# Kernel tuning notes

Measured on AMD Instinct MI355X. Metric: run time of the kernel, lower is better.

Reference implementation:

```python
import math
import jax, jax.numpy as jnp
import numpy as np

B, H, T, N, DV = 2, 8, 2048, 512, 128
THETA = 2.0 ** 16
TWO_PI = 2.0 * math.pi


def _get_freqs(n, theta):
    # quantize(arange(n), q=2): floor(t/2)*2, so each pair shares a frequency
    t = np.floor(np.arange(n, dtype=np.float32) / 2.0) * 2.0
    return (1.0 / theta ** (t / n) / TWO_PI).astype(np.float32)


def setup_inputs() -> dict:
    key = jax.random.key(0)
    k1, k2 = jax.random.split(key)
    Q = jax.random.normal(k1, (B, H, T, N), dtype=jnp.float32)
    V = jax.random.normal(k2, (B, H, T, DV), dtype=jnp.float32)
    freqs = jnp.asarray(_get_freqs(N, THETA)).reshape(1, 1, 1, N)
    return {"Q": Q, "V": V, "freqs": freqs}


def _rotate_half_interleaved(v):
    # stack((-v[..., 1::2], v[..., ::2]), -1).reshape(v.shape)
    v2 = v.reshape(*v.shape[:-1], -1, 2)
    rot = jnp.stack((-v2[..., 1], v2[..., 0]), axis=-1)
    return rot.reshape(v.shape)


def reference(Q, V, freqs):
    t = Q.shape[2]
    # phases: [1,1,T,N]
    phases = jnp.arange(t, dtype=jnp.float32).reshape(1, 1, t, 1) * freqs
    phases = (phases % 1.0) * TWO_PI
    cos, sin = jnp.cos(phases), jnp.sin(phases)
    QR = Q * cos + _rotate_half_interleaved(Q) * sin  # KR = QR (K is Q)
    scores = jnp.einsum('bhtn,bhsn->bhts', QR, QR)
    scores = jnp.tril(scores, k=-1)  # strictly lower triangular, no softmax
    return jnp.einsum('bhts,bhsd->bhtd', scores, V)
```

## Files before the change

### kernel.cpp

```cpp
#include <hip/hip_runtime.h>
#include <hip/hip_bf16.h>
#include <stdint.h>

#define T_DIM 2048
#define N_DIM 512
#define DV_DIM 128
#define NH 16

typedef __bf16 bf16x8 __attribute__((ext_vector_type(8)));
typedef float f32x4 __attribute__((ext_vector_type(4)));
typedef float f32x2 __attribute__((ext_vector_type(2)));
typedef unsigned int u32x2 __attribute__((ext_vector_type(2)));
typedef unsigned int u32x4 __attribute__((ext_vector_type(4)));

__device__ __forceinline__ unsigned bf16rne(float x) {
  unsigned u = __builtin_bit_cast(unsigned, x);
  return (u + 0x7FFFu + ((u >> 16) & 1u)) >> 16;
}

__device__ __forceinline__ void load_lds16(const void* g, void* l) {
  __builtin_amdgcn_global_load_lds((const __attribute__((address_space(1))) void*)g,
                                   (__attribute__((address_space(3))) void*)l, 16, 0, 0);
}

__global__ __launch_bounds__(256, 2)
void prep_kernel(const float* __restrict__ Q, const float* __restrict__ freqs,
                 const float* __restrict__ V,
                 unsigned int* __restrict__ qrOut,
                 unsigned int* __restrict__ qrTOut,
                 unsigned short* __restrict__ vt32) {
  __shared__ unsigned int smem32[2112];
  const int bid = blockIdx.x;
  const int tid = threadIdx.x;

  if (bid < 4096) {
    auto tile32 = reinterpret_cast<unsigned int(*)[33]>(smem32);
    const unsigned short* tile16 = reinterpret_cast<const unsigned short*>(smem32);
    const int k = bid >> 3;
    const int bh = (bid & 7) + 8 * (k & 1);
    const int rest = k >> 1;
    const int tt = rest >> 3;
    const int nn = rest & 7;
    const int t0 = tt * 64, n0 = nn * 64;

    const int c2 = tid & 31;
    const int r0 = tid >> 5;
    const float f = freqs[n0 + 2 * c2];

    const float* src = Q + ((size_t)bh * T_DIM + t0) * N_DIM + n0 + 2 * c2;
    f32x2 qv[8];
#pragma unroll
    for (int it = 0; it < 8; ++it)
      qv[it] = *(const f32x2*)(src + (size_t)(it * 8 + r0) * N_DIM);

    unsigned int* qrb = qrOut + ((size_t)bh * T_DIM + t0) * 256 + (n0 >> 1) + c2;
#pragma unroll
    for (int it = 0; it < 8; ++it) {
      int r = it * 8 + r0;
      float ph = (float)(t0 + r) * f;
      ph = ph - floorf(ph);
      float sn = __builtin_amdgcn_sinf(ph);
      float cn = __builtin_amdgcn_cosf(ph);
      unsigned lo = bf16rne(qv[it].x * cn - qv[it].y * sn);
      unsigned hi = bf16rne(qv[it].y * cn + qv[it].x * sn);
      unsigned pk = lo | (hi << 16);
      qrb[(size_t)r * 256] = pk;
      tile32[r][c2] = pk;
    }
    __syncthreads();
    unsigned int* dstb = qrTOut + ((size_t)bh * N_DIM + n0) * 1024 + (t0 >> 1);
#pragma unroll
    for (int it = 0; it < 8; ++it) {
      int slot = it * 256 + tid;
      int rn = slot >> 5;
      int c2r = slot & 31;
      unsigned lo = tile16[(2 * c2r) * 66 + rn];
      unsigned hi = tile16[(2 * c2r + 1) * 66 + rn];
      dstb[(size_t)rn * 1024 + c2r] = lo | (hi << 16);
    }
  } else {
    auto tile = reinterpret_cast<unsigned short(*)[128]>(smem32);
    const int vb = bid - 4096;
    const int bh = (vb & 7) + 8 * ((vb >> 3) & 1);
    const int sb = vb >> 4;
    const float* src = V + ((size_t)bh * T_DIM + sb * 32) * DV_DIM;
    f32x4 vv[4];
#pragma unroll
    for (int i = 0; i < 4; ++i)
      vv[i] = *(const f32x4*)(src + (size_t)(i * 1024 + tid * 4));
#pragma unroll
    for (int i = 0; i < 4; ++i) {
      int idx4 = i * 256 + tid;
      int row = idx4 >> 5;
      int col4 = idx4 & 31;
      u32x2 pk;
      pk[0] = bf16rne(vv[i][0]) | (bf16rne(vv[i][1]) << 16);
      pk[1] = bf16rne(vv[i][2]) | (bf16rne(vv[i][3]) << 16);
      *(u32x2*)&tile[row][col4 * 4] = pk;
    }
    __syncthreads();
    unsigned short* dst = vt32 + ((size_t)bh * 64 + sb) * 4096;
#pragma unroll
    for (int jj = 0; jj < 2; ++jj) {
      int j = jj * 256 + tid;
      int df = j >> 6, ln = j & 63;
      int lh2 = ln & 15, lg2 = ln >> 4;
      unsigned short tmp[8];
#pragma unroll
      for (int i = 0; i < 8; ++i) tmp[i] = tile[8 * lg2 + i][16 * df + lh2];
      *(u32x4*)(dst + j * 8) = *(u32x4*)tmp;
    }
  }
}

__global__ __launch_bounds__(256, 1)
void hprefix_kernel(const unsigned short* __restrict__ qrT,
                    const unsigned short* __restrict__ vt,
                    unsigned short* __restrict__ H) {
  const int bid = blockIdx.x;
  const int bh = (bid & 7) + 8 * ((bid >> 3) & 1);
  const int slab = bid >> 4;
  const int nsl = slab >> 2;
  const int dsl = slab & 3;
  const int tid = threadIdx.x;
  const int w = tid >> 6;
  const int lane = tid & 63;
  const int lh = lane & 15, lg = lane >> 4;

  const unsigned short* qrT_h = qrT + (size_t)bh * (N_DIM * T_DIM);
  const unsigned short* vt_h = vt + (size_t)bh * (64 * 4096);
  unsigned short* H_h = H + (size_t)bh * (16 * 65536);

  const f32x4 fzero = {0.f, 0.f, 0.f, 0.f};
  f32x4 acc00 = fzero, acc01 = fzero, acc10 = fzero, acc11 = fzero;

  for (int ch = 0; ch < 16; ++ch) {
#pragma unroll
    for (int nf = 0; nf < 2; ++nf)
#pragma unroll
      for (int dfl = 0; dfl < 2; ++dfl) {
        const f32x4 a = (nf == 0) ? (dfl == 0 ? acc00 : acc01)
                                  : (dfl == 0 ? acc10 : acc11);
        int nloc = w * 32 + nf * 16 + 4 * lg;
        int nblk = nsl * 4 + (nloc >> 5);
        int lg2 = (nloc >> 3) & 3;
        int i0 = nloc & 7;
        int df = dsl * 2 + dfl;
        int slot = df * 64 + lg2 * 16 + lh;
        u32x2 pk;
        pk[0] = bf16rne(a[0]) | (bf16rne(a[1]) << 16);
        pk[1] = bf16rne(a[2]) | (bf16rne(a[3]) << 16);
        *(u32x2*)(H_h + (size_t)ch * 65536 + nblk * 4096 + slot * 8 + i0) = pk;
      }
#pragma unroll
    for (int ks = 0; ks < 4; ++ks) {
      u32x4 a0, a1, b0, b1;
      {
        const unsigned short* pa = qrT_h + (size_t)(nsl * 128 + w * 32 + lh) * T_DIM
                                   + ch * 128 + ks * 32 + lg * 8;
        a0 = *(const u32x4*)pa;
        a1 = *(const u32x4*)(pa + 16 * T_DIM);
        const unsigned short* pb = vt_h + (size_t)(ch * 4 + ks) * 4096
                                   + ((dsl * 2) * 64 + lane) * 8;
        b0 = *(const u32x4*)pb;
        b1 = *(const u32x4*)(pb + 512);
      }
      acc00 = __builtin_amdgcn_mfma_f32_16x16x32_bf16(__builtin_bit_cast(bf16x8, a0), __builtin_bit_cast(bf16x8, b0), acc00, 0, 0, 0);
      acc01 = __builtin_amdgcn_mfma_f32_16x16x32_bf16(__builtin_bit_cast(bf16x8, a0), __builtin_bit_cast(bf16x8, b1), acc01, 0, 0, 0);
      acc10 = __builtin_amdgcn_mfma_f32_16x16x32_bf16(__builtin_bit_cast(bf16x8, a1), __builtin_bit_cast(bf16x8, b0), acc10, 0, 0, 0);
      acc11 = __builtin_amdgcn_mfma_f32_16x16x32_bf16(__builtin_bit_cast(bf16x8, a1), __builtin_bit_cast(bf16x8, b1), acc11, 0, 0, 0);
    }
  }
}

__global__ __launch_bounds__(512, 1)
void chunk_kernel(const unsigned short* __restrict__ qr,
                  const unsigned short* __restrict__ vt,
                  const unsigned short* __restrict__ H,
                  float* __restrict__ out) {
  __shared__ unsigned short kh_lds[2][16384];
  __shared__ unsigned short p_lds[8 * 2048];

  const int tid = threadIdx.x;
  const int w = tid >> 6;
  const int lane = tid & 63;
  const int lh = lane & 15, lg = lane >> 4;

  const int bid = blockIdx.x;
  const int head = (bid & 7) + 8 * ((bid >> 3) & 1);
  const int ch = bid >> 4;

  const unsigned short* qr_h = qr + (size_t)head * (T_DIM * N_DIM);
  const unsigned short* vt_h = vt + (size_t)head * (64 * 4096);
  const unsigned short* H_c = H + ((size_t)head * 16 + ch) * 65536;
  float* out_h = out + (size_t)head * (T_DIM * DV_DIM);

  const int tq = w * 16;
  const int tb = ch * 128 + tq;
  const int nsb = (w >> 1) + 1;

  u32x4 qf[16];
  {
    const unsigned short* pq = qr_h + (size_t)(tb + lh) * N_DIM + lg * 8;
#pragma unroll
    for (int ks = 0; ks < 16; ++ks) qf[ks] = *(const u32x4*)(pq + ks * 32);
  }

  int koff[4];
#pragma unroll
  for (int it = 0; it < 4; ++it) {
    int j = it * 512 + tid;
    int f = j >> 6, l = j & 63;
    int st = f >> 4, ks = f & 15;
    koff[it] = (st * 16 + (l & 15)) * 1024 + ks * 64 + (l >> 4) * 16;
  }
  auto stageK = [&](int sb, int buf) {
    const char* kb = (const char*)qr_h + ((size_t)ch * 128 + sb * 32) * 1024;
#pragma unroll
    for (int it = 0; it < 4; ++it)
      load_lds16(kb + koff[it], (char*)&kh_lds[buf][0] + (it * 512 + tid) * 16);
  };
  auto stageH = [&](int q, int buf) {
#pragma unroll
    for (int it = 0; it < 4; ++it) {
      int s = it * 512 + tid;
      int nb = s >> 7;
      int dfp = (s >> 6) & 1;
      int l = s & 63;
      const unsigned short* src = H_c + nb * 4096 + (2 * q + dfp) * 512 + l * 8;
      load_lds16(src, (char*)&kh_lds[buf][0] + s * 16);
    }
  };

  stageK(0, 0);
  stageK(1, 1);

  const f32x4 fzero = {0.f, 0.f, 0.f, 0.f};
  f32x4 o[8];
#pragma unroll
  for (int df = 0; df < 8; ++df) o[df] = fzero;

  for (int sb = 0; sb < 4; ++sb) {
    asm volatile("s_waitcnt vmcnt(4)" ::: "memory");
    __builtin_amdgcn_s_barrier();
    __builtin_amdgcn_sched_barrier(0);

    if (sb < nsb) {
      f32x4 sA = fzero, sB = fzero;
      const unsigned short* kbuf = &kh_lds[sb & 1][0];
#pragma unroll
      for (int ks = 0; ks < 16; ++ks) {
        bf16x8 kf0 = *(const bf16x8*)(kbuf + ks * 512 + lane * 8);
        bf16x8 kf1 = *(const bf16x8*)(kbuf + (16 + ks) * 512 + lane * 8);
        bf16x8 qb = __builtin_bit_cast(bf16x8, qf[ks]);
        sA = __builtin_amdgcn_mfma_f32_16x16x32_bf16(kf0, qb, sA, 0, 0, 0);
        sB = __builtin_amdgcn_mfma_f32_16x16x32_bf16(kf1, qb, sB, 0, 0, 0);
      }
      const int tloc = tq + lh;
#pragma unroll
      for (int r = 0; r < 4; ++r) {
        if (sb * 32 + 4 * lg + r >= tloc) sA[r] = 0.f;
        if (sb * 32 + 16 + 4 * lg + r >= tloc) sB[r] = 0.f;
      }
      u32x2 pkA, pkB;
      pkA[0] = bf16rne(sA[0]) | (bf16rne(sA[1]) << 16);
      pkA[1] = bf16rne(sA[2]) | (bf16rne(sA[3]) << 16);
      pkB[0] = bf16rne(sB[0]) | (bf16rne(sB[1]) << 16);
      pkB[1] = bf16rne(sB[2]) | (bf16rne(sB[3]) << 16);
      const int sa_in = 4 * lg;
      const int sb_in = 16 + 4 * lg;
      *(u32x2*)&p_lds[w * 2048 + sb * 512 + ((sa_in >> 3) * 16 + lh) * 8 + (sa_in & 7)] = pkA;
      *(u32x2*)&p_lds[w * 2048 + sb * 512 + ((sb_in >> 3) * 16 + lh) * 8 + (sb_in & 7)] = pkB;
    }

    asm volatile("s_waitcnt lgkmcnt(0)" ::: "memory");
    __builtin_amdgcn_sched_barrier(0);
    __builtin_amdgcn_s_barrier();

    if (sb == 0) stageK(2, 0);
    else if (sb == 1) stageK(3, 1);
    else if (sb == 2) stageH(0, 0);
  }
  stageH(1, 1);

  for (int f = 0; f < nsb; ++f) {
    bf16x8 pa = *(const bf16x8*)&p_lds[w * 2048 + f * 512 + lane * 8];
    const unsigned short* vb = vt_h + (size_t)(ch * 4 + f) * 4096 + lane * 8;
#pragma unroll
    for (int df = 0; df < 8; ++df) {
      bf16x8 vf = *(const bf16x8*)(vb + df * 512);
      o[df] = __builtin_amdgcn_mfma_f32_16x16x32_bf16(pa, vf, o[df], 0, 0, 0);
    }
  }

  for (int q = 0; q < 4; ++q) {
    if (q < 3) asm volatile("s_waitcnt vmcnt(4)" ::: "memory");
    else       asm volatile("s_waitcnt vmcnt(0)" ::: "memory");
    __builtin_amdgcn_s_barrier();
    __builtin_amdgcn_sched_barrier(0);

    const unsigned short* hbuf = &kh_lds[q & 1][0];
#pragma unroll
    for (int ks = 0; ks < 16; ++ks) {
      bf16x8 qa = __builtin_bit_cast(bf16x8, qf[ks]);
      bf16x8 hf0 = *(const bf16x8*)(hbuf + ks * 1024 + lane * 8);
      bf16x8 hf1 = *(const bf16x8*)(hbuf + ks * 1024 + 512 + lane * 8);
      o[2 * q] = __builtin_amdgcn_mfma_f32_16x16x32_bf16(qa, hf0, o[2 * q], 0, 0, 0);
      o[2 * q + 1] = __builtin_amdgcn_mfma_f32_16x16x32_bf16(qa, hf1, o[2 * q + 1], 0, 0, 0);
    }

    asm volatile("s_waitcnt lgkmcnt(0)" ::: "memory");
    __builtin_amdgcn_sched_barrier(0);
    __builtin_amdgcn_s_barrier();

    if (q < 2) stageH(q + 2, q & 1);
  }

  float* ob = out_h + (size_t)(tb + 4 * lg) * DV_DIM + lh;
#pragma unroll
  for (int df = 0; df < 8; ++df)
#pragma unroll
    for (int r = 0; r < 4; ++r)
      ob[(size_t)r * DV_DIM + df * 16] = o[df][r];
}

extern "C" void kernel_launch(void* const* d_in, const int* in_sizes, int n_in,
                              void* d_out, int out_size, void* d_ws, size_t ws_size,
                              hipStream_t stream) {
  const float* Q = (const float*)d_in[0];
  const float* V = (const float*)d_in[1];
  const float* freqs = (const float*)d_in[2];
  float* out = (float*)d_out;

  unsigned short* qr = (unsigned short*)d_ws;
  unsigned short* qrT = qr + (size_t)16777216;
  unsigned short* vt = qrT + (size_t)16777216;
  unsigned short* H = vt + (size_t)4194304;

  hipLaunchKernelGGL(prep_kernel, dim3(5120), dim3(256), 0, stream,
                     Q, freqs, V, (unsigned int*)qr, (unsigned int*)qrT, vt);
  hipLaunchKernelGGL(hprefix_kernel, dim3(256), dim3(256), 0, stream, qrT, vt, H);
  hipLaunchKernelGGL(chunk_kernel, dim3(256), dim3(512), 0, stream, qr, vt, H, out);
}
```

Measured before the change: 77.89 us.

## Drop transposed QR buffer; transpose QR tiles through LDS inside hprefix kernel

```diff
diff --git a/kernel.cpp b/kernel.cpp
--- a/kernel.cpp
+++ b/kernel.cpp
@@ -27,15 +27,12 @@
 void prep_kernel(const float* __restrict__ Q, const float* __restrict__ freqs,
                  const float* __restrict__ V,
                  unsigned int* __restrict__ qrOut,
-                 unsigned int* __restrict__ qrTOut,
                  unsigned short* __restrict__ vt32) {
   __shared__ unsigned int smem32[2112];
   const int bid = blockIdx.x;
   const int tid = threadIdx.x;
 
   if (bid < 4096) {
-    auto tile32 = reinterpret_cast<unsigned int(*)[33]>(smem32);
-    const unsigned short* tile16 = reinterpret_cast<const unsigned short*>(smem32);
     const int k = bid >> 3;
     const int bh = (bid & 7) + 8 * (k & 1);
     const int rest = k >> 1;
@@ -63,20 +60,7 @@
       float cn = __builtin_amdgcn_cosf(ph);
       unsigned lo = bf16rne(qv[it].x * cn - qv[it].y * sn);
       unsigned hi = bf16rne(qv[it].y * cn + qv[it].x * sn);
-      unsigned pk = lo | (hi << 16);
-      qrb[(size_t)r * 256] = pk;
-      tile32[r][c2] = pk;
-    }
-    __syncthreads();
-    unsigned int* dstb = qrTOut + ((size_t)bh * N_DIM + n0) * 1024 + (t0 >> 1);
-#pragma unroll
-    for (int it = 0; it < 8; ++it) {
-      int slot = it * 256 + tid;
-      int rn = slot >> 5;
-      int c2r = slot & 31;
-      unsigned lo = tile16[(2 * c2r) * 66 + rn];
-      unsigned hi = tile16[(2 * c2r + 1) * 66 + rn];
-      dstb[(size_t)rn * 1024 + c2r] = lo | (hi << 16);
+      qrb[(size_t)r * 256] = lo | (hi << 16);
     }
   } else {
     auto tile = reinterpret_cast<unsigned short(*)[128]>(smem32);
@@ -114,9 +98,10 @@
 }
 
 __global__ __launch_bounds__(256, 1)
-void hprefix_kernel(const unsigned short* __restrict__ qrT,
+void hprefix_kernel(const unsigned short* __restrict__ qr,
                     const unsigned short* __restrict__ vt,
                     unsigned short* __restrict__ H) {
+  __shared__ unsigned short tlds[128 * 136];
   const int bid = blockIdx.x;
   const int bh = (bid & 7) + 8 * ((bid >> 3) & 1);
   const int slab = bid >> 4;
@@ -127,12 +112,14 @@
   const int lane = tid & 63;
   const int lh = lane & 15, lg = lane >> 4;
 
-  const unsigned short* qrT_h = qrT + (size_t)bh * (N_DIM * T_DIM);
+  const unsigned short* qr_h = qr + (size_t)bh * (T_DIM * N_DIM);
   const unsigned short* vt_h = vt + (size_t)bh * (64 * 4096);
   unsigned short* H_h = H + (size_t)bh * (16 * 65536);
 
   const f32x4 fzero = {0.f, 0.f, 0.f, 0.f};
   f32x4 acc00 = fzero, acc01 = fzero, acc10 = fzero, acc11 = fzero;
+
+  const int n0g = w * 32 + lh;
 
   for (int ch = 0; ch < 16; ++ch) {
 #pragma unroll
@@ -153,23 +140,39 @@
         *(u32x2*)(H_h + (size_t)ch * 65536 + nblk * 4096 + slot * 8 + i0) = pk;
       }
 #pragma unroll
+    for (int it = 0; it < 8; ++it) {
+      int slot = it * 256 + tid;
+      int t = slot >> 4;
+      int n8 = slot & 15;
+      u32x4 v = *(const u32x4*)(qr_h + (size_t)(ch * 128 + t) * N_DIM + nsl * 128 + n8 * 8);
+      *(u32x4*)&tlds[t * 136 + n8 * 8] = v;
+    }
+    __syncthreads();
+#pragma unroll
     for (int ks = 0; ks < 4; ++ks) {
-      u32x4 a0, a1, b0, b1;
+      const int tcol = ks * 32 + lg * 8;
+      const int gb = tcol * 136 + n0g;
+      u32x4 A0, A1;
+#pragma unroll
+      for (int p = 0; p < 4; ++p) {
+        A0[p] = (unsigned)tlds[gb + (2 * p) * 136]
+              | ((unsigned)tlds[gb + (2 * p + 1) * 136] << 16);
+        A1[p] = (unsigned)tlds[gb + (2 * p) * 136 + 16]
+              | ((unsigned)tlds[gb + (2 * p + 1) * 136 + 16] << 16);
+      }
+      u32x4 b0, b1;
       {
-        const unsigned short* pa = qrT_h + (size_t)(nsl * 128 + w * 32 + lh) * T_DIM
-                                   + ch * 128 + ks * 32 + lg * 8;
-        a0 = *(const u32x4*)pa;
-        a1 = *(const u32x4*)(pa + 16 * T_DIM);
         const unsigned short* pb = vt_h + (size_t)(ch * 4 + ks) * 4096
                                    + ((dsl * 2) * 64 + lane) * 8;
         b0 = *(const u32x4*)pb;
         b1 = *(const u32x4*)(pb + 512);
       }
-      acc00 = __builtin_amdgcn_mfma_f32_16x16x32_bf16(__builtin_bit_cast(bf16x8, a0), __builtin_bit_cast(bf16x8, b0), acc00, 0, 0, 0);
-      acc01 = __builtin_amdgcn_mfma_f32_16x16x32_bf16(__builtin_bit_cast(bf16x8, a0), __builtin_bit_cast(bf16x8, b1), acc01, 0, 0, 0);
-      acc10 = __builtin_amdgcn_mfma_f32_16x16x32_bf16(__builtin_bit_cast(bf16x8, a1), __builtin_bit_cast(bf16x8, b0), acc10, 0, 0, 0);
-      acc11 = __builtin_amdgcn_mfma_f32_16x16x32_bf16(__builtin_bit_cast(bf16x8, a1), __builtin_bit_cast(bf16x8, b1), acc11, 0, 0, 0);
-    }
+      acc00 = __builtin_amdgcn_mfma_f32_16x16x32_bf16(__builtin_bit_cast(bf16x8, A0), __builtin_bit_cast(bf16x8, b0), acc00, 0, 0, 0);
+      acc01 = __builtin_amdgcn_mfma_f32_16x16x32_bf16(__builtin_bit_cast(bf16x8, A0), __builtin_bit_cast(bf16x8, b1), acc01, 0, 0, 0);
+      acc10 = __builtin_amdgcn_mfma_f32_16x16x32_bf16(__builtin_bit_cast(bf16x8, A1), __builtin_bit_cast(bf16x8, b0), acc10, 0, 0, 0);
+      acc11 = __builtin_amdgcn_mfma_f32_16x16x32_bf16(__builtin_bit_cast(bf16x8, A1), __builtin_bit_cast(bf16x8, b1), acc11, 0, 0, 0);
+    }
+    __syncthreads();
   }
 }
 
@@ -333,12 +336,11 @@
   float* out = (float*)d_out;
 
   unsigned short* qr = (unsigned short*)d_ws;
-  unsigned short* qrT = qr + (size_t)16777216;
-  unsigned short* vt = qrT + (size_t)16777216;
+  unsigned short* vt = qr + (size_t)16777216;
   unsigned short* H = vt + (size_t)4194304;
 
   hipLaunchKernelGGL(prep_kernel, dim3(5120), dim3(256), 0, stream,
-                     Q, freqs, V, (unsigned int*)qr, (unsigned int*)qrT, vt);
-  hipLaunchKernelGGL(hprefix_kernel, dim3(256), dim3(256), 0, stream, qrT, vt, H);
+                     Q, freqs, V, (unsigned int*)qr, vt);
+  hipLaunchKernelGGL(hprefix_kernel, dim3(256), dim3(256), 0, stream, qr, vt, H);
   hipLaunchKernelGGL(chunk_kernel, dim3(256), dim3(512), 0, stream, qr, vt, H, out);
 }
```

Result: slower. 125.8 us (+61.5%).
